# Performance work log

Measured on AMD Instinct MI355X. Metric: run time of the kernel, lower is better.

## Reference

```python
import jax, jax.numpy as jnp
import numpy as np

RNN_HID = 64
INPUT_DIM = 35
SEQ_LEN = 48
BATCH = 4096


def setup_inputs() -> dict:
    key = jax.random.key(0)
    ks = jax.random.split(key, 16)
    x_t = jax.random.normal(ks[0], (BATCH, SEQ_LEN, INPUT_DIM), jnp.float32)
    masks = (jax.random.uniform(ks[1], (BATCH, SEQ_LEN, INPUT_DIM)) > 0.2).astype(jnp.float32)
    deltas = jax.random.uniform(ks[2], (BATCH, SEQ_LEN, INPUT_DIM), jnp.float32)
    evals = jax.random.normal(ks[3], (BATCH, SEQ_LEN, INPUT_DIM), jnp.float32)
    eval_masks = (jax.random.uniform(ks[4], (BATCH, SEQ_LEN, INPUT_DIM)) > 0.8).astype(jnp.float32)
    is_train = jnp.ones((BATCH,), jnp.float32)

    in_sz = INPUT_DIM * 2  # LSTMCell input = concat(x_c, m)
    s_lstm = 1.0 / np.sqrt(RNN_HID)
    # torch LSTMCell params: W_ih [4H, in], W_hh [4H, H], b_ih [4H], b_hh [4H]
    W_ih = jax.random.uniform(ks[5], (4 * RNN_HID, in_sz), jnp.float32, -s_lstm, s_lstm)
    W_hh = jax.random.uniform(ks[6], (4 * RNN_HID, RNN_HID), jnp.float32, -s_lstm, s_lstm)
    b_ih = jax.random.uniform(ks[7], (4 * RNN_HID,), jnp.float32, -s_lstm, s_lstm)
    b_hh = jax.random.uniform(ks[8], (4 * RNN_HID,), jnp.float32, -s_lstm, s_lstm)
    W_reg = jax.random.uniform(ks[9], (INPUT_DIM, RNN_HID), jnp.float32, -s_lstm, s_lstm)
    b_reg = jax.random.uniform(ks[10], (INPUT_DIM,), jnp.float32, -s_lstm, s_lstm)
    # TemporalDecay: W [RNN_HID, input_dim], b [RNN_HID]
    W_td = jax.random.uniform(ks[11], (RNN_HID, INPUT_DIM), jnp.float32, -s_lstm, s_lstm)
    b_td = jax.random.uniform(ks[12], (RNN_HID,), jnp.float32, -s_lstm, s_lstm)
    # out Linear(RNN_HID -> 1)
    W_out = jax.random.uniform(ks[13], (1, RNN_HID), jnp.float32, -s_lstm, s_lstm)
    b_out = jax.random.uniform(ks[14], (1,), jnp.float32, -s_lstm, s_lstm)
    return {
        'x_t': x_t, 'masks': masks, 'deltas': deltas, 'evals': evals,
        'eval_masks': eval_masks, 'is_train': is_train,
        'W_ih': W_ih, 'W_hh': W_hh, 'b_ih': b_ih, 'b_hh': b_hh,
        'W_reg': W_reg, 'b_reg': b_reg, 'W_td': W_td, 'b_td': b_td,
        'W_out': W_out, 'b_out': b_out,
    }


def _lstm_cell(inp, h, c, W_ih, W_hh, b_ih, b_hh):
    # gates ordered i, f, g, o as in torch.nn.LSTMCell
    gates = inp @ W_ih.T + h @ W_hh.T + b_ih + b_hh  # [B, 4H]
    i, f, g, o = jnp.split(gates, 4, axis=-1)
    i = jax.nn.sigmoid(i)
    f = jax.nn.sigmoid(f)
    g = jnp.tanh(g)
    o = jax.nn.sigmoid(o)
    c_new = f * c + i * g
    h_new = o * jnp.tanh(c_new)
    return h_new, c_new


def reference(x_t, masks, deltas, evals, eval_masks, is_train,
              W_ih, W_hh, b_ih, b_hh, W_reg, b_reg, W_td, b_td, W_out, b_out):
    B, T, D = x_t.shape
    h0 = jnp.zeros((B, RNN_HID), x_t.dtype)
    c0 = jnp.zeros((B, RNN_HID), x_t.dtype)

    def step(carry, xs):
        h, c, x_loss = carry
        x, m, d = xs  # each [B, D]
        x_hat = h @ W_reg.T + b_reg
        x_c = m * x + (1.0 - m) * x_hat
        x_loss = x_loss + jnp.sum(jnp.abs(x - x_hat) * m) / (jnp.sum(m) + 1e-5)
        inputs = jnp.concatenate([x_c, m], axis=1)  # [B, 2D]
        # temporal decay (computed as in original, result unused)
        gamma = jnp.exp(-jax.nn.relu(d @ W_td.T + b_td))
        h, c = _lstm_cell(inputs, h, c, W_ih, W_hh, b_ih, b_hh)
        return (h, c, x_loss), x_c

    xs = (jnp.swapaxes(x_t, 0, 1), jnp.swapaxes(masks, 0, 1), jnp.swapaxes(deltas, 0, 1))
    (h, c, x_loss), imp = jax.lax.scan(step, (h0, c0, jnp.float32(0.0)), xs)
    imputations = jnp.swapaxes(imp, 0, 1)  # [B, T, D]
    y_h = jax.nn.sigmoid(h @ W_out.T + b_out)
    loss = x_loss / T  # y_loss == 0
    return loss, y_h, imputations
```

## Files before the change

kernel.cpp:

```cpp
#include <hip/hip_runtime.h>
#include <stdint.h>

#define B_    4096
#define T_    48
#define D_    35
#define KROW  168
#define BT    16
#define ROWEL (T_ * D_)
#define L2E   1.44269504f

typedef float f32x4 __attribute__((ext_vector_type(4)));
typedef short bf16x8 __attribute__((ext_vector_type(8)));

__device__ __forceinline__ uint32_t fbits(float x) { union { float f; uint32_t u; } v; v.f = x; return v.u; }
__device__ __forceinline__ float bitsf(uint32_t u) { union { uint32_t u; float f; } v; v.u = u; return v.f; }
__device__ __forceinline__ float bf2f(unsigned short b) { return bitsf(((uint32_t)b) << 16); }
__device__ __forceinline__ unsigned short f2bf_rne(float x) {
    uint32_t u = fbits(x);
    return (unsigned short)((u + 0x7fffu + ((u >> 16) & 1u)) >> 16);
}
__device__ __forceinline__ float rcp_(float x)  { return __builtin_amdgcn_rcpf(x); }
__device__ __forceinline__ float exp2_(float x) { return __builtin_amdgcn_exp2f(x); }


__global__ __launch_bounds__(256, 1)
void brits_main(const float* __restrict__ x_t, const float* __restrict__ masks,
                const float* __restrict__ W_ih, const float* __restrict__ W_hh,
                const float* __restrict__ b_ih, const float* __restrict__ b_hh,
                const float* __restrict__ W_reg, const float* __restrict__ b_reg,
                const float* __restrict__ W_out, const float* __restrict__ b_out,
                float* __restrict__ ws, float* __restrict__ out)
{
    __shared__ __align__(16) unsigned short Abuf[2][BT * KROW];
    __shared__ __align__(16) unsigned short stash[BT * ROWEL];
    __shared__ unsigned long long mbits[BT * T_];
    __shared__ float lsum[T_ * 3 * 64];
    __shared__ float wout[65];

    const int tid    = threadIdx.x;
    const int lane   = tid & 63;
    const int w      = tid >> 6;
    const int g      = lane >> 4;
    const int cc     = lane & 15;
    const int batch0 = blockIdx.x * BT;
    const int u      = w * 16 + cc;

    for (int i = tid; i < BT * KROW; i += 256) ((uint32_t*)Abuf)[i] = 0;
    if (tid < 65) wout[tid] = (tid < 64) ? W_out[tid] : b_out[0];

    for (int i = tid; i < BT * (ROWEL / 8); i += 256) {
        const int r = i / 210;
        const int o = (i - r * 210) * 8;
        const float* xp = x_t   + (size_t)(batch0 + r) * ROWEL + o;
        const float* mp = masks + (size_t)(batch0 + r) * ROWEL + o;
        float xv[8], mv[8];
        *(float4*)&xv[0] = *(const float4*)xp; *(float4*)&xv[4] = *(const float4*)(xp + 4);
        *(float4*)&mv[0] = *(const float4*)mp; *(float4*)&mv[4] = *(const float4*)(mp + 4);
        unsigned short pk[8];
        #pragma unroll
        for (int k = 0; k < 8; ++k) pk[k] = f2bf_rne(mv[k] * xv[k]);
        *(uint4*)&stash[r * ROWEL + o] = *(const uint4*)pk;
    }
    for (int p = tid; p < BT * T_; p += 256) {
        const int r = p / T_, t = p - r * T_;
        const float* mp = masks + (size_t)(batch0 + r) * ROWEL + t * D_;
        unsigned long long bits = 0;
        for (int d = 0; d < D_; ++d) bits |= (unsigned long long)(mp[d] != 0.0f) << d;
        mbits[p] = bits;
    }

    bf16x8 Wf[4][5];
    #pragma unroll
    for (int G = 0; G < 4; ++G) {
        const int n = G * 64 + u;
        #pragma unroll
        for (int kk = 0; kk < 5; ++kk) {
            bf16x8 v;
            #pragma unroll
            for (int i = 0; i < 8; ++i) {
                const int k = kk * 32 + 8 * g + i;
                float f = 0.f;
                if (k < 70)                  f = W_ih[n * 70 + k];
                else if (k >= 72 && k < 136) f = W_hh[n * 64 + (k - 72)];
                v[i] = (short)f2bf_rne(f);
            }
            Wf[G][kk] = v;
        }
    }
    bf16x8 Wr0, Wr1;
    {
        const bool ok = (w < 3) && (u < 35);
        #pragma unroll
        for (int i = 0; i < 8; ++i) {
            Wr0[i] = (short)(ok ? f2bf_rne(W_reg[u * 64 + 8 * g + i])      : 0);
            Wr1[i] = (short)(ok ? f2bf_rne(W_reg[u * 64 + 32 + 8 * g + i]) : 0);
        }
    }
    const float brg = ((w < 3) && (u < 35)) ? b_reg[u] : 0.f;
    const float bIs = -(b_ih[u]       + b_hh[u])       * L2E;
    const float bFs = -(b_ih[64 + u]  + b_hh[64 + u])  * L2E;
    const float bGs = -(b_ih[128 + u] + b_hh[128 + u]) * 2.f * L2E;
    const float bOs = -(b_ih[192 + u] + b_hh[192 + u]) * L2E;
    __syncthreads();

    const bool pl = (w < 3) && (u < 35);
    unsigned long long PM[4] = {0, 0, 0, 0};
    uint32_t xmr[4] = {0, 0, 0, 0};
    if (pl) {
        #pragma unroll
        for (int j = 0; j < 4; ++j) {
            const int row = 4 * g + j;
            unsigned long long pm = 0;
            for (int t = 0; t < T_; ++t)
                pm |= ((mbits[row * T_ + t] >> u) & 1ull) << t;
            PM[j] = pm;
            xmr[j] = stash[row * ROWEL + u];
            Abuf[0][row * KROW + 35 + u] = (pm & 1ull) ? (unsigned short)0x3F80 : (unsigned short)0;
        }
    }
    __syncthreads();

    float c_reg[4] = {0.f, 0.f, 0.f, 0.f};

    for (int t = 0; t < T_; ++t) {
        unsigned short* A  = Abuf[t & 1];
        unsigned short* An = Abuf[(t + 1) & 1];

        bf16x8 ah0 = *(const bf16x8*)&A[cc * KROW + 72  + 8 * g];
        bf16x8 ah1 = *(const bf16x8*)&A[cc * KROW + 104 + 8 * g];
        bf16x8 a2  = *(const bf16x8*)&A[cc * KROW + 64  + 8 * g];
        bf16x8 a3  = *(const bf16x8*)&A[cc * KROW + 96  + 8 * g];
        bf16x8 a4  = *(const bf16x8*)&A[cc * KROW + 128 + 8 * g];

        f32x4 gI = {0,0,0,0}, gF = {0,0,0,0}, gG = {0,0,0,0}, gO = {0,0,0,0};
        gI = __builtin_amdgcn_mfma_f32_16x16x32_bf16(a2, Wf[0][2], gI, 0, 0, 0);
        gF = __builtin_amdgcn_mfma_f32_16x16x32_bf16(a2, Wf[1][2], gF, 0, 0, 0);
        gG = __builtin_amdgcn_mfma_f32_16x16x32_bf16(a2, Wf[2][2], gG, 0, 0, 0);
        gO = __builtin_amdgcn_mfma_f32_16x16x32_bf16(a2, Wf[3][2], gO, 0, 0, 0);
        gI = __builtin_amdgcn_mfma_f32_16x16x32_bf16(a3, Wf[0][3], gI, 0, 0, 0);
        gF = __builtin_amdgcn_mfma_f32_16x16x32_bf16(a3, Wf[1][3], gF, 0, 0, 0);
        gG = __builtin_amdgcn_mfma_f32_16x16x32_bf16(a3, Wf[2][3], gG, 0, 0, 0);
        gO = __builtin_amdgcn_mfma_f32_16x16x32_bf16(a3, Wf[3][3], gO, 0, 0, 0);
        gI = __builtin_amdgcn_mfma_f32_16x16x32_bf16(a4, Wf[0][4], gI, 0, 0, 0);
        gF = __builtin_amdgcn_mfma_f32_16x16x32_bf16(a4, Wf[1][4], gF, 0, 0, 0);
        gG = __builtin_amdgcn_mfma_f32_16x16x32_bf16(a4, Wf[2][4], gG, 0, 0, 0);
        gO = __builtin_amdgcn_mfma_f32_16x16x32_bf16(a4, Wf[3][4], gO, 0, 0, 0);

        if (w < 3) {
            f32x4 p0 = {0,0,0,0};
            p0 = __builtin_amdgcn_mfma_f32_16x16x32_bf16(ah0, Wr0, p0, 0, 0, 0);
            p0 = __builtin_amdgcn_mfma_f32_16x16x32_bf16(ah1, Wr1, p0, 0, 0, 0);
            float lnum = 0.f;
            if (u < 35) {
                #pragma unroll
                for (int j = 0; j < 4; ++j) {
                    const int row = 4 * g + j;
                    const float xh = p0[j] + brg;
                    const float xm = bf2f((unsigned short)xmr[j]);
                    const uint32_t mb = (uint32_t)(PM[j] >> t) & 1u;
                    lnum += mb ? fabsf(xm - xh) : 0.f;
                    const unsigned short xc16 = mb ? (unsigned short)xmr[j] : f2bf_rne(xh);
                    A[row * KROW + u] = xc16;
                    An[row * KROW + 35 + u] =
                        ((PM[j] >> (t + 1)) & 1ull) ? (unsigned short)0x3F80 : (unsigned short)0;
                    stash[row * ROWEL + t * D_ + u] = xc16;
                }
            }
            lsum[(t * 3 + w) * 64 + lane] = lnum;
        }
        __syncthreads();

        bf16x8 a0 = *(const bf16x8*)&A[cc * KROW + 0  + 8 * g];
        bf16x8 a1 = *(const bf16x8*)&A[cc * KROW + 32 + 8 * g];
        gI = __builtin_amdgcn_mfma_f32_16x16x32_bf16(a0, Wf[0][0], gI, 0, 0, 0);
        gF = __builtin_amdgcn_mfma_f32_16x16x32_bf16(a0, Wf[1][0], gF, 0, 0, 0);
        gG = __builtin_amdgcn_mfma_f32_16x16x32_bf16(a0, Wf[2][0], gG, 0, 0, 0);
        gO = __builtin_amdgcn_mfma_f32_16x16x32_bf16(a0, Wf[3][0], gO, 0, 0, 0);
        gI = __builtin_amdgcn_mfma_f32_16x16x32_bf16(a1, Wf[0][1], gI, 0, 0, 0);
        gF = __builtin_amdgcn_mfma_f32_16x16x32_bf16(a1, Wf[1][1], gF, 0, 0, 0);
        gG = __builtin_amdgcn_mfma_f32_16x16x32_bf16(a1, Wf[2][1], gG, 0, 0, 0);
        gO = __builtin_amdgcn_mfma_f32_16x16x32_bf16(a1, Wf[3][1], gO, 0, 0, 0);

        if (pl && t + 1 < T_) {
            #pragma unroll
            for (int j = 0; j < 4; ++j)
                xmr[j] = stash[(4 * g + j) * ROWEL + (t + 1) * D_ + u];
        }

        #pragma unroll
        for (int j = 0; j < 4; ++j) {
            const float iv = rcp_(1.f + exp2_(fmaf(gI[j], -L2E,       bIs)));
            const float fv = rcp_(1.f + exp2_(fmaf(gF[j], -L2E,       bFs)));
            const float gv = fmaf(2.f, rcp_(1.f + exp2_(fmaf(gG[j], -2.f * L2E, bGs))), -1.f);
            const float ov = rcp_(1.f + exp2_(fmaf(gO[j], -L2E,       bOs)));
            const float cn = fmaf(fv, c_reg[j], iv * gv);
            c_reg[j] = cn;
            const float th = fmaf(2.f, rcp_(1.f + exp2_(cn * (-2.f * L2E))), -1.f);
            An[(4 * g + j) * KROW + 72 + u] = (unsigned short)(fbits(ov * th) >> 16);
        }
        __syncthreads();
    }

    if (tid < T_) {
        const int t = tid;
        float num = 0.f;
        for (int i = 0; i < 192; ++i) num += lsum[t * 192 + i];
        float den = 0.f;
        for (int r = 0; r < BT; ++r) den += (float)__popcll(mbits[r * T_ + t]);
        atomicAdd(&ws[t * 8 + (blockIdx.x & 7)], num);
        atomicAdd(&ws[(T_ + t) * 8 + (blockIdx.x & 7)], den);
    }

    if (w == 1) {
        float p = 0.f;
        #pragma unroll
        for (int k = 0; k < 16; ++k)
            p += bf2f(Abuf[0][cc * KROW + 72 + 16 * g + k]) * wout[16 * g + k];
        p += __shfl_xor(p, 16, 64);
        p += __shfl_xor(p, 32, 64);
        if (lane < 16) out[1 + batch0 + cc] = rcp_(1.f + exp2_(-(p + wout[64]) * L2E));
    }

    for (int i = tid; i < BT * ROWEL; i += 256) {
        const int r = i / ROWEL;
        const int o = i - r * ROWEL;
        out[1 + B_ + (size_t)(batch0 + r) * ROWEL + o] = bf2f(stash[i]);
    }
}

__global__ void post_kernel(const float* __restrict__ ws, float* __restrict__ out)
{
    const int t = threadIdx.x;
    float v = 0.f;
    if (t < T_) {
        float num = 0.f, den = 0.f;
        #pragma unroll
        for (int s = 0; s < 8; ++s) {
            num += ws[t * 8 + s];
            den += ws[(T_ + t) * 8 + s];
        }
        v = num / (den + 1e-5f);
    }
    #pragma unroll
    for (int off = 1; off < 64; off <<= 1) v += __shfl_xor(v, off, 64);
    if (t == 0) out[0] = v * (1.0f / T_);
}

extern "C" void kernel_launch(void* const* d_in, const int* in_sizes, int n_in,
                              void* d_out, int out_size, void* d_ws, size_t ws_size,
                              hipStream_t stream) {
    const float* x_t   = (const float*)d_in[0];
    const float* masks = (const float*)d_in[1];
    const float* W_ih  = (const float*)d_in[6];
    const float* W_hh  = (const float*)d_in[7];
    const float* b_ih  = (const float*)d_in[8];
    const float* b_hh  = (const float*)d_in[9];
    const float* W_reg = (const float*)d_in[10];
    const float* b_reg = (const float*)d_in[11];
    const float* W_out = (const float*)d_in[14];
    const float* b_out = (const float*)d_in[15];
    float* out = (float*)d_out;
    float* ws  = (float*)d_ws;

    hipMemsetAsync(ws, 0, 2 * T_ * 8 * sizeof(float), stream);
    brits_main<<<B_ / BT, 256, 0, stream>>>(x_t, masks, W_ih, W_hh, b_ih, b_hh,
                                            W_reg, b_reg, W_out, b_out, ws, out);
    post_kernel<<<1, 64, 0, stream>>>(ws, out);
}
```

Measured before the change: 87.55 us.

## Split LSTM gate and regression work into separate wavefronts per block

Doubles the block to 512 threads and gives the LSTM gate MFMAs and activations to waves 0-3 and the W_reg regression/imputation path to waves 4-6, instead of having waves 0-2 do both. The aim is to take the regression and imputation work off the critical path of the gate computation within each timestep. The cost is more threads per block, which may lower occupancy, and an idle wave 7. The two per-step barriers and the serial step dependency are unchanged, so any overlap is limited.

Measured after the change: 86.19 us (median of 2 runs). About the same (-1.6%).

```diff
diff --git a/kernel.cpp b/kernel.cpp
--- a/kernel.cpp
+++ b/kernel.cpp
@@ -5,25 +5,25 @@
 #define T_    48
 #define D_    35
 #define KROW  168
-#define BT    16
 #define ROWEL (T_ * D_)
 #define L2E   1.44269504f
 
 typedef float f32x4 __attribute__((ext_vector_type(4)));
 typedef short bf16x8 __attribute__((ext_vector_type(8)));
 
-__device__ __forceinline__ uint32_t fbits(float x) { union { float f; uint32_t u; } v; v.f = x; return v.u; }
-__device__ __forceinline__ float bitsf(uint32_t u) { union { uint32_t u; float f; } v; v.u = u; return v.f; }
-__device__ __forceinline__ float bf2f(unsigned short b) { return bitsf(((uint32_t)b) << 16); }
-__device__ __forceinline__ unsigned short f2bf_rne(float x) {
-    uint32_t u = fbits(x);
-    return (unsigned short)((u + 0x7fffu + ((u >> 16) & 1u)) >> 16);
-}
-__device__ __forceinline__ float rcp_(float x)  { return __builtin_amdgcn_rcpf(x); }
-__device__ __forceinline__ float exp2_(float x) { return __builtin_amdgcn_exp2f(x); }
-
-
-__global__ __launch_bounds__(256, 1)
+static __device__ __forceinline__ uint32_t fbits(float x){union{float f;uint32_t u;}v;v.f=x;return v.u;}
+static __device__ __forceinline__ float bitsf(uint32_t u){union{uint32_t u;float f;}v;v.u=u;return v.f;}
+static __device__ __forceinline__ float bf2f(unsigned short b){return bitsf(((uint32_t)b)<<16);}
+static __device__ __forceinline__ unsigned short f2bf_rne(float x){
+    uint32_t u=fbits(x); return (unsigned short)((u+0x7fffu+((u>>16)&1u))>>16);
+}
+static __device__ __forceinline__ float rcp_(float x){return __builtin_amdgcn_rcpf(x);}
+static __device__ __forceinline__ float exp2_(float x){return __builtin_amdgcn_exp2f(x);}
+
+#define MFMA __builtin_amdgcn_mfma_f32_16x16x32_bf16
+
+
+__global__ __launch_bounds__(512, 1)
 void brits_main(const float* __restrict__ x_t, const float* __restrict__ masks,
                 const float* __restrict__ W_ih, const float* __restrict__ W_hh,
                 const float* __restrict__ b_ih, const float* __restrict__ b_hh,
@@ -31,9 +31,9 @@
                 const float* __restrict__ W_out, const float* __restrict__ b_out,
                 float* __restrict__ ws, float* __restrict__ out)
 {
-    __shared__ __align__(16) unsigned short Abuf[2][BT * KROW];
-    __shared__ __align__(16) unsigned short stash[BT * ROWEL];
-    __shared__ unsigned long long mbits[BT * T_];
+    __shared__ __align__(16) unsigned short Abuf[2][16 * KROW];
+    __shared__ __align__(16) unsigned short stash[16 * ROWEL];
+    __shared__ unsigned long long mbits[16 * T_];
     __shared__ float lsum[T_ * 3 * 64];
     __shared__ float wout[65];
 
@@ -42,13 +42,14 @@
     const int w      = tid >> 6;
     const int g      = lane >> 4;
     const int cc     = lane & 15;
-    const int batch0 = blockIdx.x * BT;
-    const int u      = w * 16 + cc;
-
-    for (int i = tid; i < BT * KROW; i += 256) ((uint32_t*)Abuf)[i] = 0;
+    const int batch0 = blockIdx.x * 16;
+    const int u      = (w & 3) * 16 + cc;
+    const int u2     = (w - 4) * 16 + cc;
+
+    for (int i = tid; i < 16 * KROW; i += 512) ((uint32_t*)Abuf)[i] = 0;
     if (tid < 65) wout[tid] = (tid < 64) ? W_out[tid] : b_out[0];
 
-    for (int i = tid; i < BT * (ROWEL / 8); i += 256) {
+    for (int i = tid; i < 16 * 210; i += 512) {
         const int r = i / 210;
         const int o = (i - r * 210) * 8;
         const float* xp = x_t   + (size_t)(batch0 + r) * ROWEL + o;
@@ -61,49 +62,53 @@
         for (int k = 0; k < 8; ++k) pk[k] = f2bf_rne(mv[k] * xv[k]);
         *(uint4*)&stash[r * ROWEL + o] = *(const uint4*)pk;
     }
-    for (int p = tid; p < BT * T_; p += 256) {
+    for (int p = tid; p < 16 * T_; p += 512) {
         const int r = p / T_, t = p - r * T_;
         const float* mp = masks + (size_t)(batch0 + r) * ROWEL + t * D_;
         unsigned long long bits = 0;
-        for (int d = 0; d < D_; ++d) bits |= (unsigned long long)(mp[d] != 0.0f) << d;
+        for (int d = 0; d < D_; ++d) bits |= (unsigned long long)(mp[d] != 0.f) << d;
         mbits[p] = bits;
     }
 
     bf16x8 Wf[4][5];
-    #pragma unroll
-    for (int G = 0; G < 4; ++G) {
-        const int n = G * 64 + u;
-        #pragma unroll
-        for (int kk = 0; kk < 5; ++kk) {
-            bf16x8 v;
+    float bIs = 0.f, bFs = 0.f, bGs = 0.f, bOs = 0.f;
+    if (w < 4) {
+        #pragma unroll
+        for (int G = 0; G < 4; ++G) {
+            const int n = G * 64 + u;
             #pragma unroll
-            for (int i = 0; i < 8; ++i) {
-                const int k = kk * 32 + 8 * g + i;
-                float f = 0.f;
-                if (k < 70)                  f = W_ih[n * 70 + k];
-                else if (k >= 72 && k < 136) f = W_hh[n * 64 + (k - 72)];
-                v[i] = (short)f2bf_rne(f);
+            for (int kc = 0; kc < 5; ++kc) {
+                bf16x8 v;
+                #pragma unroll
+                for (int i = 0; i < 8; ++i) {
+                    const int k = kc * 32 + 8 * g + i;
+                    float f = 0.f;
+                    if (k < 70)                  f = W_ih[n * 70 + k];
+                    else if (k >= 72 && k < 136) f = W_hh[n * 64 + (k - 72)];
+                    v[i] = (short)f2bf_rne(f);
+                }
+                Wf[G][kc] = v;
             }
-            Wf[G][kk] = v;
-        }
-    }
-    bf16x8 Wr0, Wr1;
-    {
-        const bool ok = (w < 3) && (u < 35);
+        }
+        bIs = -(b_ih[u]       + b_hh[u])       * L2E;
+        bFs = -(b_ih[64 + u]  + b_hh[64 + u])  * L2E;
+        bGs = -(b_ih[128 + u] + b_hh[128 + u]) * 2.f * L2E;
+        bOs = -(b_ih[192 + u] + b_hh[192 + u]) * L2E;
+    }
+    bf16x8 Wr0 = {0,0,0,0,0,0,0,0}, Wr1 = {0,0,0,0,0,0,0,0};
+    float brg = 0.f;
+    const bool pw = (w >= 4) && (w < 7);
+    const bool pl = pw && (u2 < 35);
+    if (pl) {
         #pragma unroll
         for (int i = 0; i < 8; ++i) {
-            Wr0[i] = (short)(ok ? f2bf_rne(W_reg[u * 64 + 8 * g + i])      : 0);
-            Wr1[i] = (short)(ok ? f2bf_rne(W_reg[u * 64 + 32 + 8 * g + i]) : 0);
-        }
-    }
-    const float brg = ((w < 3) && (u < 35)) ? b_reg[u] : 0.f;
-    const float bIs = -(b_ih[u]       + b_hh[u])       * L2E;
-    const float bFs = -(b_ih[64 + u]  + b_hh[64 + u])  * L2E;
-    const float bGs = -(b_ih[128 + u] + b_hh[128 + u]) * 2.f * L2E;
-    const float bOs = -(b_ih[192 + u] + b_hh[192 + u]) * L2E;
+            Wr0[i] = (short)f2bf_rne(W_reg[u2 * 64 + 8 * g + i]);
+            Wr1[i] = (short)f2bf_rne(W_reg[u2 * 64 + 32 + 8 * g + i]);
+        }
+        brg = b_reg[u2];
+    }
     __syncthreads();
 
-    const bool pl = (w < 3) && (u < 35);
     unsigned long long PM[4] = {0, 0, 0, 0};
     uint32_t xmr[4] = {0, 0, 0, 0};
     if (pl) {
@@ -112,46 +117,46 @@
             const int row = 4 * g + j;
             unsigned long long pm = 0;
             for (int t = 0; t < T_; ++t)
-                pm |= ((mbits[row * T_ + t] >> u) & 1ull) << t;
+                pm |= ((mbits[row * T_ + t] >> u2) & 1ull) << t;
             PM[j] = pm;
-            xmr[j] = stash[row * ROWEL + u];
-            Abuf[0][row * KROW + 35 + u] = (pm & 1ull) ? (unsigned short)0x3F80 : (unsigned short)0;
+            xmr[j] = stash[row * ROWEL + u2];
+            Abuf[0][row * KROW + 35 + u2] = (pm & 1ull) ? (unsigned short)0x3F80 : (unsigned short)0;
         }
     }
     __syncthreads();
 
-    float c_reg[4] = {0.f, 0.f, 0.f, 0.f};
+    float c_[4] = {0.f, 0.f, 0.f, 0.f};
 
     for (int t = 0; t < T_; ++t) {
         unsigned short* A  = Abuf[t & 1];
         unsigned short* An = Abuf[(t + 1) & 1];
 
-        bf16x8 ah0 = *(const bf16x8*)&A[cc * KROW + 72  + 8 * g];
-        bf16x8 ah1 = *(const bf16x8*)&A[cc * KROW + 104 + 8 * g];
-        bf16x8 a2  = *(const bf16x8*)&A[cc * KROW + 64  + 8 * g];
-        bf16x8 a3  = *(const bf16x8*)&A[cc * KROW + 96  + 8 * g];
-        bf16x8 a4  = *(const bf16x8*)&A[cc * KROW + 128 + 8 * g];
-
         f32x4 gI = {0,0,0,0}, gF = {0,0,0,0}, gG = {0,0,0,0}, gO = {0,0,0,0};
-        gI = __builtin_amdgcn_mfma_f32_16x16x32_bf16(a2, Wf[0][2], gI, 0, 0, 0);
-        gF = __builtin_amdgcn_mfma_f32_16x16x32_bf16(a2, Wf[1][2], gF, 0, 0, 0);
-        gG = __builtin_amdgcn_mfma_f32_16x16x32_bf16(a2, Wf[2][2], gG, 0, 0, 0);
-        gO = __builtin_amdgcn_mfma_f32_16x16x32_bf16(a2, Wf[3][2], gO, 0, 0, 0);
-        gI = __builtin_amdgcn_mfma_f32_16x16x32_bf16(a3, Wf[0][3], gI, 0, 0, 0);
-        gF = __builtin_amdgcn_mfma_f32_16x16x32_bf16(a3, Wf[1][3], gF, 0, 0, 0);
-        gG = __builtin_amdgcn_mfma_f32_16x16x32_bf16(a3, Wf[2][3], gG, 0, 0, 0);
-        gO = __builtin_amdgcn_mfma_f32_16x16x32_bf16(a3, Wf[3][3], gO, 0, 0, 0);
-        gI = __builtin_amdgcn_mfma_f32_16x16x32_bf16(a4, Wf[0][4], gI, 0, 0, 0);
-        gF = __builtin_amdgcn_mfma_f32_16x16x32_bf16(a4, Wf[1][4], gF, 0, 0, 0);
-        gG = __builtin_amdgcn_mfma_f32_16x16x32_bf16(a4, Wf[2][4], gG, 0, 0, 0);
-        gO = __builtin_amdgcn_mfma_f32_16x16x32_bf16(a4, Wf[3][4], gO, 0, 0, 0);
-
-        if (w < 3) {
+
+        if (w < 4) {
+            bf16x8 a2 = *(const bf16x8*)&A[cc * KROW + 64  + 8 * g];
+            bf16x8 a3 = *(const bf16x8*)&A[cc * KROW + 96  + 8 * g];
+            bf16x8 a4 = *(const bf16x8*)&A[cc * KROW + 128 + 8 * g];
+            gI = MFMA(a2, Wf[0][2], gI, 0,0,0);
+            gF = MFMA(a2, Wf[1][2], gF, 0,0,0);
+            gG = MFMA(a2, Wf[2][2], gG, 0,0,0);
+            gO = MFMA(a2, Wf[3][2], gO, 0,0,0);
+            gI = MFMA(a3, Wf[0][3], gI, 0,0,0);
+            gF = MFMA(a3, Wf[1][3], gF, 0,0,0);
+            gG = MFMA(a3, Wf[2][3], gG, 0,0,0);
+            gO = MFMA(a3, Wf[3][3], gO, 0,0,0);
+            gI = MFMA(a4, Wf[0][4], gI, 0,0,0);
+            gF = MFMA(a4, Wf[1][4], gF, 0,0,0);
+            gG = MFMA(a4, Wf[2][4], gG, 0,0,0);
+            gO = MFMA(a4, Wf[3][4], gO, 0,0,0);
+        } else if (pw) {
+            bf16x8 ah0 = *(const bf16x8*)&A[cc * KROW + 72  + 8 * g];
+            bf16x8 ah1 = *(const bf16x8*)&A[cc * KROW + 104 + 8 * g];
             f32x4 p0 = {0,0,0,0};
-            p0 = __builtin_amdgcn_mfma_f32_16x16x32_bf16(ah0, Wr0, p0, 0, 0, 0);
-            p0 = __builtin_amdgcn_mfma_f32_16x16x32_bf16(ah1, Wr1, p0, 0, 0, 0);
+            p0 = MFMA(ah0, Wr0, p0, 0,0,0);
+            p0 = MFMA(ah1, Wr1, p0, 0,0,0);
             float lnum = 0.f;
-            if (u < 35) {
+            if (u2 < 35) {
                 #pragma unroll
                 for (int j = 0; j < 4; ++j) {
                     const int row = 4 * g + j;
@@ -160,43 +165,42 @@
                     const uint32_t mb = (uint32_t)(PM[j] >> t) & 1u;
                     lnum += mb ? fabsf(xm - xh) : 0.f;
                     const unsigned short xc16 = mb ? (unsigned short)xmr[j] : f2bf_rne(xh);
-                    A[row * KROW + u] = xc16;
-                    An[row * KROW + 35 + u] =
+                    A[row * KROW + u2] = xc16;
+                    An[row * KROW + 35 + u2] =
                         ((PM[j] >> (t + 1)) & 1ull) ? (unsigned short)0x3F80 : (unsigned short)0;
-                    stash[row * ROWEL + t * D_ + u] = xc16;
+                    stash[row * ROWEL + t * D_ + u2] = xc16;
                 }
             }
-            lsum[(t * 3 + w) * 64 + lane] = lnum;
+            lsum[(t * 3 + (w - 4)) * 64 + lane] = lnum;
         }
         __syncthreads();
 
-        bf16x8 a0 = *(const bf16x8*)&A[cc * KROW + 0  + 8 * g];
-        bf16x8 a1 = *(const bf16x8*)&A[cc * KROW + 32 + 8 * g];
-        gI = __builtin_amdgcn_mfma_f32_16x16x32_bf16(a0, Wf[0][0], gI, 0, 0, 0);
-        gF = __builtin_amdgcn_mfma_f32_16x16x32_bf16(a0, Wf[1][0], gF, 0, 0, 0);
-        gG = __builtin_amdgcn_mfma_f32_16x16x32_bf16(a0, Wf[2][0], gG, 0, 0, 0);
-        gO = __builtin_amdgcn_mfma_f32_16x16x32_bf16(a0, Wf[3][0], gO, 0, 0, 0);
-        gI = __builtin_amdgcn_mfma_f32_16x16x32_bf16(a1, Wf[0][1], gI, 0, 0, 0);
-        gF = __builtin_amdgcn_mfma_f32_16x16x32_bf16(a1, Wf[1][1], gF, 0, 0, 0);
-        gG = __builtin_amdgcn_mfma_f32_16x16x32_bf16(a1, Wf[2][1], gG, 0, 0, 0);
-        gO = __builtin_amdgcn_mfma_f32_16x16x32_bf16(a1, Wf[3][1], gO, 0, 0, 0);
-
-        if (pl && t + 1 < T_) {
+        if (w < 4) {
+            bf16x8 a0 = *(const bf16x8*)&A[cc * KROW + 0  + 8 * g];
+            bf16x8 a1 = *(const bf16x8*)&A[cc * KROW + 32 + 8 * g];
+            gI = MFMA(a0, Wf[0][0], gI, 0,0,0);
+            gF = MFMA(a0, Wf[1][0], gF, 0,0,0);
+            gG = MFMA(a0, Wf[2][0], gG, 0,0,0);
+            gO = MFMA(a0, Wf[3][0], gO, 0,0,0);
+            gI = MFMA(a1, Wf[0][1], gI, 0,0,0);
+            gF = MFMA(a1, Wf[1][1], gF, 0,0,0);
+            gG = MFMA(a1, Wf[2][1], gG, 0,0,0);
+            gO = MFMA(a1, Wf[3][1], gO, 0,0,0);
+            #pragma unroll
+            for (int j = 0; j < 4; ++j) {
+                const float iv = rcp_(1.f + exp2_(fmaf(gI[j], -L2E,       bIs)));
+                const float fv = rcp_(1.f + exp2_(fmaf(gF[j], -L2E,       bFs)));
+                const float gv = fmaf(2.f, rcp_(1.f + exp2_(fmaf(gG[j], -2.f * L2E, bGs))), -1.f);
+                const float ov = rcp_(1.f + exp2_(fmaf(gO[j], -L2E,       bOs)));
+                const float cn = fmaf(fv, c_[j], iv * gv);
+                c_[j] = cn;
+                const float th = fmaf(2.f, rcp_(1.f + exp2_(cn * (-2.f * L2E))), -1.f);
+                An[(4 * g + j) * KROW + 72 + u] = (unsigned short)(fbits(ov * th) >> 16);
+            }
+        } else if (pl && t + 1 < T_) {
             #pragma unroll
             for (int j = 0; j < 4; ++j)
-                xmr[j] = stash[(4 * g + j) * ROWEL + (t + 1) * D_ + u];
-        }
-
-        #pragma unroll
-        for (int j = 0; j < 4; ++j) {
-            const float iv = rcp_(1.f + exp2_(fmaf(gI[j], -L2E,       bIs)));
-            const float fv = rcp_(1.f + exp2_(fmaf(gF[j], -L2E,       bFs)));
-            const float gv = fmaf(2.f, rcp_(1.f + exp2_(fmaf(gG[j], -2.f * L2E, bGs))), -1.f);
-            const float ov = rcp_(1.f + exp2_(fmaf(gO[j], -L2E,       bOs)));
-            const float cn = fmaf(fv, c_reg[j], iv * gv);
-            c_reg[j] = cn;
-            const float th = fmaf(2.f, rcp_(1.f + exp2_(cn * (-2.f * L2E))), -1.f);
-            An[(4 * g + j) * KROW + 72 + u] = (unsigned short)(fbits(ov * th) >> 16);
+                xmr[j] = stash[(4 * g + j) * ROWEL + (t + 1) * D_ + u2];
         }
         __syncthreads();
     }
@@ -206,7 +210,7 @@
         float num = 0.f;
         for (int i = 0; i < 192; ++i) num += lsum[t * 192 + i];
         float den = 0.f;
-        for (int r = 0; r < BT; ++r) den += (float)__popcll(mbits[r * T_ + t]);
+        for (int r = 0; r < 16; ++r) den += (float)__popcll(mbits[r * T_ + t]);
         atomicAdd(&ws[t * 8 + (blockIdx.x & 7)], num);
         atomicAdd(&ws[(T_ + t) * 8 + (blockIdx.x & 7)], den);
     }
@@ -221,7 +225,7 @@
         if (lane < 16) out[1 + batch0 + cc] = rcp_(1.f + exp2_(-(p + wout[64]) * L2E));
     }
 
-    for (int i = tid; i < BT * ROWEL; i += 256) {
+    for (int i = tid; i < 16 * ROWEL; i += 512) {
         const int r = i / ROWEL;
         const int o = i - r * ROWEL;
         out[1 + B_ + (size_t)(batch0 + r) * ROWEL + o] = bf2f(stash[i]);
@@ -263,7 +267,7 @@
     float* ws  = (float*)d_ws;
 
     hipMemsetAsync(ws, 0, 2 * T_ * 8 * sizeof(float), stream);
-    brits_main<<<B_ / BT, 256, 0, stream>>>(x_t, masks, W_ih, W_hh, b_ih, b_hh,
+    brits_main<<<B_ / 16, 512, 0, stream>>>(x_t, masks, W_ih, W_hh, b_ih, b_hh,
                                             W_reg, b_reg, W_out, b_out, ws, out);
     post_kernel<<<1, 64, 0, stream>>>(ws, out);
 }
```
